# Optimization experiments

Measured on AMD Instinct MI355X. Metric: run time of the kernel, lower is better.

Reference implementation:

```python
import jax, jax.numpy as jnp
import numpy as np

B = 16384        # batch size
D = 128          # embedding dim == ln_bot[-1]
N_EMB = 26       # number of sparse tables
VOCAB = 50000    # rows per table
LN_BOT = [13, 512, 256, 128]
LN_TOP = [479, 1024, 1024, 512, 1]
# triangular indices matching: li=[i for i in range(ni) for j in range(i)] (offset=0, no self-interaction)
LI, LJ = np.tril_indices(N_EMB + 1, -1)


def _init_linear(key, n_in, n_out):
    kw, kb = jax.random.split(key)
    lim = 1.0 / np.sqrt(n_in)
    W = jax.random.uniform(kw, (n_in, n_out), minval=-lim, maxval=lim, dtype=jnp.float32)
    b = jax.random.uniform(kb, (n_out,), minval=-lim, maxval=lim, dtype=jnp.float32)
    return W, b


def setup_inputs() -> dict:
    key = jax.random.key(0)
    ks = jax.random.split(key, 3 + len(LN_BOT) - 1 + len(LN_TOP) - 1)
    inp = {
        "dense_x": jax.random.normal(ks[0], (B, LN_BOT[0]), dtype=jnp.float32),
        "indices": jax.random.randint(ks[1], (N_EMB, B), 0, VOCAB),
        "emb_tables": jax.random.normal(ks[2], (N_EMB, VOCAB, D), dtype=jnp.float32) * 0.01,
    }
    k = 3
    for i in range(len(LN_BOT) - 1):
        W, b = _init_linear(ks[k], LN_BOT[i], LN_BOT[i + 1]); k += 1
        inp[f"bot_W{i}"], inp[f"bot_b{i}"] = W, b
    for i in range(len(LN_TOP) - 1):
        W, b = _init_linear(ks[k], LN_TOP[i], LN_TOP[i + 1]); k += 1
        inp[f"top_W{i}"], inp[f"top_b{i}"] = W, b
    return inp


def reference(dense_x, indices, emb_tables,
              bot_W0, bot_b0, bot_W1, bot_b1, bot_W2, bot_b2,
              top_W0, top_b0, top_W1, top_b1, top_W2, top_b2, top_W3, top_b3):
    # bottom MLP (sigmoid_bot=-1 -> all ReLU)
    x = dense_x
    for W, b in ((bot_W0, bot_b0), (bot_W1, bot_b1), (bot_W2, bot_b2)):
        x = jax.nn.relu(x @ W + b)                      # [B, 128]

    # embedding lookups (bag size 1 per table)
    emb = jax.vmap(lambda t, i: t[i])(emb_tables, indices)   # [26, B, D]
    emb = jnp.transpose(emb, (1, 0, 2))                      # [B, 26, D]

    # dot interaction
    T = jnp.concatenate([x[:, None, :], emb], axis=1)        # [B, 27, D]
    Z = jnp.einsum('bid,bjd->bij', T, T)                     # [B, 27, 27]
    Zflat = Z[:, LI, LJ]                                     # [B, 351]
    R = jnp.concatenate([x, Zflat], axis=1)                  # [B, 479]

    # top MLP (sigmoid on last layer, sigmoid_top=3)
    h = R
    for W, b in ((top_W0, top_b0), (top_W1, top_b1), (top_W2, top_b2)):
        h = jax.nn.relu(h @ W + b)
    p = jax.nn.sigmoid(h @ top_W3 + top_b3)                  # [B, 1]
    return jnp.clip(p, 0.0, 1.0)                             # loss_threshold = 0.0
```

## Files before the change

### kernel.cpp

```cpp
#include <hip/hip_runtime.h>

typedef __attribute__((ext_vector_type(8))) short short8;
typedef __attribute__((ext_vector_type(4))) float f32x4;
typedef __attribute__((ext_vector_type(16))) float f32x16;

#define B_ROWS 16384

__device__ __forceinline__ float bf2f(ushort u){ return __uint_as_float(((uint)u)<<16); }
__device__ __forceinline__ ushort f2bf(float f){
  uint u = __float_as_uint(f);
  u = u + 0x7FFFu + ((u>>16)&1u);
  return (ushort)(u>>16);
}
__device__ __forceinline__ void gload_lds16(const void* g, void* l){
  __builtin_amdgcn_global_load_lds((const __attribute__((address_space(1))) unsigned*)g,
                                   (__attribute__((address_space(3))) unsigned*)l, 16, 0, 0);
}

struct TArgs { const float* in; ushort* out; int K, N, Kp; };
struct TArgs6 { TArgs a[6]; };

__global__ __launch_bounds__(256) void transp_tiled(TArgs6 args)
{
  TArgs t = args.a[blockIdx.z];
  if (t.K == 0){
    if (blockIdx.x==0 && blockIdx.y==0)
      for (int i = threadIdx.x; i < t.N; i += 256) t.out[i] = f2bf(t.in[i]);
    return;
  }
  int k0 = blockIdx.x*32, n0 = blockIdx.y*32;
  if (k0 >= t.Kp || n0 >= t.N) return;
  __shared__ float tile[32][33];
  const int c = threadIdx.x & 31, r8 = threadIdx.x >> 5;
  #pragma unroll
  for (int p=0;p<4;p++){
    int k = k0 + r8 + p*8;
    tile[r8+p*8][c] = (k < t.K) ? t.in[(size_t)k*t.N + n0 + c] : 0.f;
  }
  __syncthreads();
  #pragma unroll
  for (int p=0;p<4;p++){
    int n = n0 + r8 + p*8;
    t.out[(size_t)n*t.Kp + k0 + c] = f2bf(tile[c][r8+p*8]);
  }
}

__global__ __launch_bounds__(256) void bot0(const float* __restrict__ x, const float* __restrict__ W,
                                            const float* __restrict__ bias, ushort* __restrict__ out)
{
  int i = blockIdx.x*256 + threadIdx.x;
  int b = i>>9, n = i&511;
  const float* xr = x + (size_t)b*13;
  float s = bias[n];
  #pragma unroll
  for (int k=0;k<13;k++) s += xr[k]*W[k*512+n];
  out[i] = f2bf(fmaxf(s,0.f));
}

template<int TM, bool RELU>
__global__ __launch_bounds__(256) void gemm_bt(const ushort* __restrict__ A,
    const ushort* __restrict__ Bt, const float* __restrict__ bias,
    ushort* __restrict__ C, int M, int N, int K, int ldc)
{
  constexpr int BM = TM*32;
  __shared__ __align__(16) ushort lA[2][BM*64];
  __shared__ __align__(16) ushort lB[2][128*64];
  const int tid = threadIdx.x;
  const int wave = tid>>6, lane = tid&63;
  const int bm = blockIdx.x*BM, bn = blockIdx.y*128;
  const int wrr = (wave>>1)*(BM/2), wcc = (wave&1)*64;
  const int lr = lane&15, lg = lane>>4;
  const int nt = K>>6;
  const int obA = wave*(TM*1024) + lane*16;
  const int obB = wave*4096 + lane*16;

  f32x4 acc[TM][4];
  #pragma unroll
  for (int m=0;m<TM;m++)
    #pragma unroll
    for (int n=0;n<4;n++)
      #pragma unroll
      for (int j=0;j<4;j++) acc[m][n][j] = 0.f;

  auto stage = [&](int buf, int kt){
    #pragma unroll
    for (int c=0;c<TM;c++){
      int o = obA + c*1024;
      int row = o>>7, colb = o&127;
      gload_lds16((const char*)A  + (((size_t)(bm+row)*K + (kt<<6))<<1) + colb, (char*)lA[buf] + o);
    }
    #pragma unroll
    for (int c=0;c<4;c++){
      int o = obB + c*1024;
      int row = o>>7, colb = o&127;
      gload_lds16((const char*)Bt + (((size_t)(bn+row)*K + (kt<<6))<<1) + colb, (char*)lB[buf] + o);
    }
  };

  stage(0, 0);
  int cur = 0;
  for (int t=0; t<nt; ++t){
    int nx = (t+1 < nt) ? t+1 : 0;
    stage(cur^1, nx);
    if constexpr (TM==4) asm volatile("s_waitcnt vmcnt(8)" ::: "memory");
    else                 asm volatile("s_waitcnt vmcnt(6)" ::: "memory");
    __builtin_amdgcn_s_barrier();
    asm volatile("" ::: "memory");
    #pragma unroll
    for (int kk=0;kk<64;kk+=32){
      short8 af[TM], bfr[4];
      const int lk = kk + lg*8;
      #pragma unroll
      for (int m=0;m<TM;m++) af[m]  = *(const short8*)&lA[cur][(wrr+m*16+lr)*64 + lk];
      #pragma unroll
      for (int n=0;n<4;n++) bfr[n] = *(const short8*)&lB[cur][(wcc+n*16+lr)*64 + lk];
      #pragma unroll
      for (int m=0;m<TM;m++)
        #pragma unroll
        for (int n=0;n<4;n++)
          acc[m][n] = __builtin_amdgcn_mfma_f32_16x16x32_bf16(af[m], bfr[n], acc[m][n], 0,0,0);
    }
    asm volatile("" ::: "memory");
    __builtin_amdgcn_s_barrier();
    cur ^= 1;
  }

  #pragma unroll
  for (int n=0;n<4;n++){
    int col = bn + wcc + n*16 + lr;
    float bv = bias[col];
    #pragma unroll
    for (int m=0;m<TM;m++){
      #pragma unroll
      for (int j=0;j<4;j++){
        int row = bm + wrr + m*16 + lg*4 + j;
        float v = acc[m][n][j] + bv;
        if (RELU) v = fmaxf(v,0.f);
        C[(size_t)row*ldc + col] = f2bf(v);
      }
    }
  }
}

template<int BN>
__global__ __launch_bounds__(512, 2) void gemm256(const ushort* __restrict__ A,
    const ushort* __restrict__ Bt, const float* __restrict__ bias,
    ushort* __restrict__ C, int K, int ldc)
{
  constexpr int  NF = BN/128;
  constexpr int  LB = BN/128;
  constexpr uint BR = (uint)BN*32u;
  constexpr uint BUFSZ = 16384u + 2u*BR;
  __shared__ __align__(16) ushort lds[2*BUFSZ];

  const int tid = threadIdx.x;
  const int wave = tid>>6, lane = tid&63;
  const uint wm = (uint)(wave>>2), wn = (uint)(wave&3);
  const uint lc = (uint)(lane&31), hi = (uint)(lane>>5);
  const int bm = blockIdx.x*256, bn = blockIdx.y*BN;
  const int nt = K>>6, niter = nt>>1;

  f32x16 acc[4][NF];
  #pragma unroll
  for (int m=0;m<4;m++)
    #pragma unroll
    for (int n=0;n<NF;n++)
      #pragma unroll
      for (int j=0;j<16;j++) acc[m][n][j] = 0.f;

  short8 bfr[2][NF];

#define STAGE(MAT, KH, TILE, SBUF) do{                                          \
    int kt_ = (TILE);                                                           \
    int ktc_ = (kt_ < nt) ? kt_ : 0;       \
    const ushort* gb_ = (MAT) ? Bt : A;                                         \
    const uint ro_ = (MAT) ? (uint)bn : (uint)bm;                               \
    const uint rb_ = (uint)(SBUF)*BUFSZ + ((MAT) ? (16384u + (uint)(KH)*BR)     \
                                                 : ((uint)(KH)*8192u));         \
    const int nl_ = (MAT) ? LB : 2;                                             \
    _Pragma("unroll")                                                           \
    for (int j_=0; j_<nl_; ++j_){                                               \
      uint lin_ = (uint)tid*16u + (uint)j_*8192u;                               \
      uint src_ = lin_ ^ (((lin_>>7)&3u)<<4);                                   \
      uint row_ = src_>>6, colb_ = src_&63u;                                    \
      const char* g_ = (const char*)gb_ +                                       \
        (((size_t)(ro_+row_)*(size_t)K + (size_t)ktc_*64 + (KH)*32)<<1) + colb_;\
      gload_lds16(g_, (char*)lds + (size_t)rb_*2 + lin_);                       \
    }                                                                           \
  }while(0)

#define PHASE(CBUF, KKH, MH, BLOAD, SMAT, SKH, STILE, SBUF, CKPT) do{           \
    const uint ab_ = (uint)(CBUF)*BUFSZ + (uint)(KKH)*8192u;                    \
    short8 af_[2][2];                                                           \
    _Pragma("unroll")                                                           \
    for (int mfl_=0; mfl_<2; ++mfl_){                                           \
      uint r_ = wm*128u + ((uint)(MH)*2u+(uint)mfl_)*32u + lc;                  \
      _Pragma("unroll")                                                         \
      for (int k2_=0; k2_<2; ++k2_){                                            \
        uint l_ = r_*64u + hi*16u + (uint)k2_*32u;                              \
        af_[mfl_][k2_] = *(const short8*)((const char*)lds + (size_t)ab_*2      \
                                   + (l_ ^ (((l_>>7)&3u)<<4)));                 \
      }                                                                         \
    }                                                                           \
    if (BLOAD){                                                                 \
      const uint bb_ = (uint)(CBUF)*BUFSZ + 16384u + (uint)(KKH)*BR;            \
      _Pragma("unroll")                                                         \
      for (int nf_=0; nf_<NF; ++nf_){                                           \
        uint r_ = wn*(uint)(BN/4) + (uint)nf_*32u + lc;                         \
        _Pragma("unroll")                                                       \
        for (int k2_=0; k2_<2; ++k2_){                                          \
          uint l_ = r_*64u + hi*16u + (uint)k2_*32u;                            \
          bfr[k2_][nf_] = *(const short8*)((const char*)lds + (size_t)bb_*2     \
                                     + (l_ ^ (((l_>>7)&3u)<<4)));               \
        }                                                                       \
      }                                                                         \
    }                                                                           \
    STAGE(SMAT, SKH, STILE, SBUF);                                              \
    asm volatile("" ::: "memory");                                              \
    __builtin_amdgcn_s_barrier();                                               \
    asm volatile("" ::: "memory");                                              \
    __builtin_amdgcn_s_setprio(1);                                              \
    _Pragma("unroll")                                                           \
    for (int mfl_=0; mfl_<2; ++mfl_)                                            \
      _Pragma("unroll")                                                         \
      for (int nf_=0; nf_<NF; ++nf_)                                            \
        _Pragma("unroll")                                                       \
        for (int k2_=0; k2_<2; ++k2_)                                           \
          acc[(MH)*2+mfl_][nf_] = __builtin_amdgcn_mfma_f32_32x32x16_bf16(      \
              af_[mfl_][k2_], bfr[k2_][nf_], acc[(MH)*2+mfl_][nf_], 0,0,0);     \
    __builtin_amdgcn_s_setprio(0);                                              \
    if (CKPT){                                                                  \
      if constexpr (LB==2) asm volatile("s_waitcnt vmcnt(4)" ::: "memory");     \
      else                 asm volatile("s_waitcnt vmcnt(3)" ::: "memory");     \
    }                                                                           \
    asm volatile("" ::: "memory");                                              \
    __builtin_amdgcn_s_barrier();                                               \
  }while(0)

  STAGE(0,0,0,0); STAGE(1,0,0,0); STAGE(0,1,0,0); STAGE(1,1,0,0);
  STAGE(0,0,1,1); STAGE(1,0,1,1);
  if constexpr (LB==2) asm volatile("s_waitcnt vmcnt(4)" ::: "memory");
  else                 asm volatile("s_waitcnt vmcnt(3)" ::: "memory");
  asm volatile("" ::: "memory");
  __builtin_amdgcn_s_barrier();

  for (int i=0; i<niter; ++i){
    const int O  = 2*i+1;
    const int E2 = 2*i+2;
    const int O2 = 2*i+3;
    PHASE(0,0,0,true , 0,1,O ,1, false);
    PHASE(0,0,1,false, 1,1,O ,1, true );
    PHASE(0,1,0,true , 0,0,E2,0, false);
    PHASE(0,1,1,false, 1,0,E2,0, true );
    PHASE(1,0,0,true , 0,1,E2,0, false);
    PHASE(1,0,1,false, 1,1,E2,0, true );
    PHASE(1,1,0,true , 0,0,O2,1, false);
    PHASE(1,1,1,false, 1,0,O2,1, true );
  }
#undef PHASE
#undef STAGE

  #pragma unroll
  for (int nf=0; nf<NF; ++nf){
    int col = bn + (int)wn*(BN/4) + nf*32 + (int)lc;
    float bv = bias[col];
    #pragma unroll
    for (int mf=0; mf<4; ++mf){
      #pragma unroll
      for (int reg=0; reg<16; ++reg){
        int row = bm + (int)wm*128 + mf*32 + (reg&3) + 8*(reg>>2) + 4*(int)hi;
        float v = acc[mf][nf][reg] + bv;
        C[(size_t)row*ldc + col] = f2bf(fmaxf(v, 0.f));
      }
    }
  }
}

__global__ __launch_bounds__(256) void interact(const int* __restrict__ idx,
    const float* __restrict__ emb, ushort* __restrict__ R)
{
  __shared__ __align__(16) ushort Tl[4][32][136];
  const int w = threadIdx.x>>6, l = threadIdx.x&63;
  const int b = blockIdx.x*4 + w;
  ushort* Rrow = R + (size_t)b*512;

  uint xv = ((const uint*)Rrow)[l];
  *(uint*)&Tl[w][0][2*l] = xv;

  int myidx = (l<26) ? idx[(size_t)l*B_ROWS + b] : 0;
  const int half = l>>5, lc = l&31;
  #pragma unroll
  for (int i=0;i<13;i++){
    const int row = 2*i + 1 + half;
    int e = __shfl(myidx, row - 1);
    const float4* rp = (const float4*)(emb + ((size_t)(row-1)*50000 + (size_t)e)*128);
    float4 v = rp[lc];
    uint2 pk;
    pk.x = (uint)f2bf(v.x) | ((uint)f2bf(v.y)<<16);
    pk.y = (uint)f2bf(v.z) | ((uint)f2bf(v.w)<<16);
    *(uint2*)&Tl[w][row][4*lc] = pk;
  }
  __syncthreads();

  f32x16 acc;
  #pragma unroll
  for (int i=0;i<16;i++) acc[i] = 0.f;
  #pragma unroll
  for (int kk=0;kk<8;kk++){
    short8 fa = *(const short8*)((const char*)&Tl[w][0][0] + (size_t)(l&31)*272 + kk*32 + (l>>5)*16);
    acc = __builtin_amdgcn_mfma_f32_32x32x16_bf16(fa, fa, acc, 0,0,0);
  }

  const int c = l&31;
  #pragma unroll
  for (int j=0;j<16;j++){
    int r = (j&3) + 8*(j>>2) + 4*(l>>5);
    if (c < r && r <= 26) Rrow[128 + r*(r-1)/2 + c] = f2bf(acc[j]);
  }
  if (l < 33) Rrow[479 + l] = 0;
}

__global__ __launch_bounds__(256) void finlayer(const ushort* __restrict__ h3,
    const ushort* __restrict__ wt, const float* __restrict__ b3, float* __restrict__ out)
{
  int w = threadIdx.x>>6, l = threadIdx.x&63;
  int b = blockIdx.x*4 + w;
  short8 hv = *(const short8*)(h3 + (size_t)b*512 + l*8);
  short8 wv = *(const short8*)(wt + l*8);
  float s = 0.f;
  #pragma unroll
  for (int j=0;j<8;j++) s += bf2f((ushort)hv[j])*bf2f((ushort)wv[j]);
  #pragma unroll
  for (int off=32; off>0; off>>=1) s += __shfl_xor(s, off);
  if (l==0){
    float h = s + b3[0];
    float p = 1.f/(1.f + expf(-h));
    out[b] = fminf(fmaxf(p, 0.f), 1.f);
  }
}

extern "C" void kernel_launch(void* const* d_in, const int* in_sizes, int n_in,
                              void* d_out, int out_size, void* d_ws, size_t ws_size,
                              hipStream_t stream)
{
  const float* dense_x = (const float*)d_in[0];
  const int*   indices = (const int*)d_in[1];
  const float* emb     = (const float*)d_in[2];
  const float* bW0 = (const float*)d_in[3];  const float* bb0 = (const float*)d_in[4];
  const float* bW1 = (const float*)d_in[5];  const float* bb1 = (const float*)d_in[6];
  const float* bW2 = (const float*)d_in[7];  const float* bb2 = (const float*)d_in[8];
  const float* tW0 = (const float*)d_in[9];  const float* tb0 = (const float*)d_in[10];
  const float* tW1 = (const float*)d_in[11]; const float* tb1 = (const float*)d_in[12];
  const float* tW2 = (const float*)d_in[13]; const float* tb2 = (const float*)d_in[14];
  const float* tW3 = (const float*)d_in[15]; const float* tb3 = (const float*)d_in[16];
  float* out = (float*)d_out;
  const int Bn = B_ROWS;

  char* ws = (char*)d_ws;
  size_t o = 0;
  auto alloc = [&](size_t bytes)->char*{ char* r = ws + o; o += (bytes + 255) & ~(size_t)255; return r; };
  ushort* wtB1 = (ushort*)alloc(256*512*2);
  ushort* wtB2 = (ushort*)alloc(128*256*2);
  ushort* wtT0 = (ushort*)alloc(1024*512*2);
  ushort* wtT1 = (ushort*)alloc((size_t)1024*1024*2);
  ushort* wtT2 = (ushort*)alloc(512*1024*2);
  ushort* wtT3 = (ushort*)alloc(512*2);
  ushort* P    = (ushort*)alloc((size_t)Bn*512*2);
  ushort* act1 = (ushort*)alloc((size_t)Bn*256*2);
  ushort* h1   = (ushort*)alloc((size_t)Bn*1024*2);
  ushort* h2   = (ushort*)alloc((size_t)Bn*1024*2);
  (void)ws_size; (void)in_sizes; (void)n_in; (void)out_size;

  TArgs6 ta;
  ta.a[0] = { bW1, wtB1, 512 , 256 , 512  };
  ta.a[1] = { bW2, wtB2, 256 , 128 , 256  };
  ta.a[2] = { tW0, wtT0, 479 , 1024, 512  };
  ta.a[3] = { tW1, wtT1, 1024, 1024, 1024 };
  ta.a[4] = { tW2, wtT2, 1024, 512 , 1024 };
  ta.a[5] = { tW3, wtT3, 0   , 512 , 0    };
  transp_tiled<<<dim3(32,32,6),256,0,stream>>>(ta);

  bot0<<<Bn*512/256,256,0,stream>>>(dense_x, bW0, bb0, P);
  gemm_bt<4,true><<<dim3(128,2),256,0,stream>>>(P,    wtB1, bb1, act1, Bn,256,512, 256);
  gemm_bt<2,true><<<dim3(256,1),256,0,stream>>>(act1, wtB2, bb2, P,    Bn,128,256, 512);

  interact<<<Bn/4,256,0,stream>>>(indices, emb, P);

  gemm256<256><<<dim3(64,4),512,0,stream>>>(P,  wtT0, tb0, h1, 512 , 1024);
  gemm256<256><<<dim3(64,4),512,0,stream>>>(h1, wtT1, tb1, h2, 1024, 1024);
  gemm256<128><<<dim3(64,4),512,0,stream>>>(h2, wtT2, tb2, P,  1024, 512);
  finlayer<<<Bn/4,256,0,stream>>>(P, wtT3, tb3, out);
}
```

Baseline: 197.0 us.

## Fuse final dot layer into last GEMM epilogue and merge prep kernels

Merges the weight-transpose kernel and the first bottom-MLP layer into one prep kernel that also zeroes a partial-sum buffer. The last top-MLP GEMM now applies bias and ReLU, multiplies by the final-layer weight, reduces across lanes and atomically adds into per-row partials. A small sigmoid kernel then finishes the output. This avoids writing and re-reading the 16384x512 activation and saves launches, at the cost of float atomics (order-dependent sums) and a shuffle reduction in the epilogue.

After: 197.2 us. No clear change (+0.1%).

```diff
diff --git a/kernel.cpp b/kernel.cpp
--- a/kernel.cpp
+++ b/kernel.cpp
@@ -18,43 +18,53 @@
 }
 
 struct TArgs { const float* in; ushort* out; int K, N, Kp; };
-struct TArgs6 { TArgs a[6]; };
-
-__global__ __launch_bounds__(256) void transp_tiled(TArgs6 args)
-{
-  TArgs t = args.a[blockIdx.z];
-  if (t.K == 0){
-    if (blockIdx.x==0 && blockIdx.y==0)
-      for (int i = threadIdx.x; i < t.N; i += 256) t.out[i] = f2bf(t.in[i]);
+struct PrepArgs {
+  const float* x; const float* W0; const float* b0; ushort* act0;
+  TArgs t[5];
+  float* partial;
+};
+
+__global__ __launch_bounds__(256) void prep(PrepArgs a)
+{
+  const int idx = blockIdx.x;
+  const int tid = threadIdx.x;
+  __shared__ float tile[32][33];
+
+  if (idx < 32768){
+    int i = idx*256 + tid;
+    int b = i>>9, n = i&511;
+    const float* xr = a.x + (size_t)b*13;
+    float s = a.b0[n];
+    #pragma unroll
+    for (int k=0;k<13;k++) s += xr[k]*a.W0[k*512+n];
+    a.act0[i] = f2bf(fmaxf(s,0.f));
     return;
   }
-  int k0 = blockIdx.x*32, n0 = blockIdx.y*32;
-  if (k0 >= t.Kp || n0 >= t.N) return;
-  __shared__ float tile[32][33];
-  const int c = threadIdx.x & 31, r8 = threadIdx.x >> 5;
+  if (idx >= 34976){
+    a.partial[(idx-34976)*256 + tid] = 0.f;
+    return;
+  }
+  int t = idx - 32768, s;
+  int kx, ny;
+  if (t < 128)            { s=0; kx=t%16; ny=t/16; }
+  else if ((t-=128) < 32) { s=1; kx=t%8 ; ny=t/8 ; }
+  else if ((t-=32) < 512) { s=2; kx=t%16; ny=t/16; }
+  else if ((t-=512)<1024) { s=3; kx=t%32; ny=t/32; }
+  else                    { s=4; kx=(t-1024)%32; ny=(t-1024)/32; }
+  TArgs ta = a.t[s];
+  int k0 = kx*32, n0 = ny*32;
+  const int c = tid & 31, r8 = tid >> 5;
   #pragma unroll
   for (int p=0;p<4;p++){
     int k = k0 + r8 + p*8;
-    tile[r8+p*8][c] = (k < t.K) ? t.in[(size_t)k*t.N + n0 + c] : 0.f;
+    tile[r8+p*8][c] = (k < ta.K) ? ta.in[(size_t)k*ta.N + n0 + c] : 0.f;
   }
   __syncthreads();
   #pragma unroll
   for (int p=0;p<4;p++){
     int n = n0 + r8 + p*8;
-    t.out[(size_t)n*t.Kp + k0 + c] = f2bf(tile[c][r8+p*8]);
-  }
-}
-
-__global__ __launch_bounds__(256) void bot0(const float* __restrict__ x, const float* __restrict__ W,
-                                            const float* __restrict__ bias, ushort* __restrict__ out)
-{
-  int i = blockIdx.x*256 + threadIdx.x;
-  int b = i>>9, n = i&511;
-  const float* xr = x + (size_t)b*13;
-  float s = bias[n];
-  #pragma unroll
-  for (int k=0;k<13;k++) s += xr[k]*W[k*512+n];
-  out[i] = f2bf(fmaxf(s,0.f));
+    ta.out[(size_t)n*ta.Kp + k0 + c] = f2bf(tile[c][r8+p*8]);
+  }
 }
 
 template<int TM, bool RELU>
@@ -142,10 +152,11 @@
   }
 }
 
-template<int BN>
+template<int BN, bool FUSE>
 __global__ __launch_bounds__(512, 2) void gemm256(const ushort* __restrict__ A,
     const ushort* __restrict__ Bt, const float* __restrict__ bias,
-    ushort* __restrict__ C, int K, int ldc)
+    ushort* __restrict__ C, int K, int ldc,
+    const float* __restrict__ w3, float* __restrict__ partial)
 {
   constexpr int  NF = BN/128;
   constexpr int  LB = BN/128;
@@ -260,17 +271,36 @@
 #undef PHASE
 #undef STAGE
 
-  #pragma unroll
-  for (int nf=0; nf<NF; ++nf){
-    int col = bn + (int)wn*(BN/4) + nf*32 + (int)lc;
+  if constexpr (FUSE){
+    int col = bn + (int)wn*(BN/4) + (int)lc;
     float bv = bias[col];
+    float wv = w3[col];
     #pragma unroll
     for (int mf=0; mf<4; ++mf){
       #pragma unroll
       for (int reg=0; reg<16; ++reg){
-        int row = bm + (int)wm*128 + mf*32 + (reg&3) + 8*(reg>>2) + 4*(int)hi;
-        float v = acc[mf][nf][reg] + bv;
-        C[(size_t)row*ldc + col] = f2bf(fmaxf(v, 0.f));
+        float v = fmaxf(acc[mf][0][reg] + bv, 0.f) * wv;
+        #pragma unroll
+        for (int off=1; off<32; off<<=1) v += __shfl_xor(v, off);
+        if (lc == 0){
+          int row = bm + (int)wm*128 + mf*32 + (reg&3) + 8*(reg>>2) + 4*(int)hi;
+          atomicAdd(&partial[row], v);
+        }
+      }
+    }
+  } else {
+    #pragma unroll
+    for (int nf=0; nf<NF; ++nf){
+      int col = bn + (int)wn*(BN/4) + nf*32 + (int)lc;
+      float bv = bias[col];
+      #pragma unroll
+      for (int mf=0; mf<4; ++mf){
+        #pragma unroll
+        for (int reg=0; reg<16; ++reg){
+          int row = bm + (int)wm*128 + mf*32 + (reg&3) + 8*(reg>>2) + 4*(int)hi;
+          float v = acc[mf][nf][reg] + bv;
+          C[(size_t)row*ldc + col] = f2bf(fmaxf(v, 0.f));
+        }
       }
     }
   }
@@ -320,23 +350,13 @@
   if (l < 33) Rrow[479 + l] = 0;
 }
 
-__global__ __launch_bounds__(256) void finlayer(const ushort* __restrict__ h3,
-    const ushort* __restrict__ wt, const float* __restrict__ b3, float* __restrict__ out)
-{
-  int w = threadIdx.x>>6, l = threadIdx.x&63;
-  int b = blockIdx.x*4 + w;
-  short8 hv = *(const short8*)(h3 + (size_t)b*512 + l*8);
-  short8 wv = *(const short8*)(wt + l*8);
-  float s = 0.f;
-  #pragma unroll
-  for (int j=0;j<8;j++) s += bf2f((ushort)hv[j])*bf2f((ushort)wv[j]);
-  #pragma unroll
-  for (int off=32; off>0; off>>=1) s += __shfl_xor(s, off);
-  if (l==0){
-    float h = s + b3[0];
-    float p = 1.f/(1.f + expf(-h));
-    out[b] = fminf(fmaxf(p, 0.f), 1.f);
-  }
+__global__ __launch_bounds__(256) void sigm(const float* __restrict__ partial,
+    const float* __restrict__ b3, float* __restrict__ out)
+{
+  int i = blockIdx.x*256 + threadIdx.x;
+  float h = partial[i] + b3[0];
+  float p = 1.f/(1.f + expf(-h));
+  out[i] = fminf(fmaxf(p, 0.f), 1.f);
 }
 
 extern "C" void kernel_launch(void* const* d_in, const int* in_sizes, int n_in,
@@ -364,30 +384,30 @@
   ushort* wtT0 = (ushort*)alloc(1024*512*2);
   ushort* wtT1 = (ushort*)alloc((size_t)1024*1024*2);
   ushort* wtT2 = (ushort*)alloc(512*1024*2);
-  ushort* wtT3 = (ushort*)alloc(512*2);
+  float*  partial = (float*)alloc(B_ROWS*4);
   ushort* P    = (ushort*)alloc((size_t)Bn*512*2);
   ushort* act1 = (ushort*)alloc((size_t)Bn*256*2);
   ushort* h1   = (ushort*)alloc((size_t)Bn*1024*2);
   ushort* h2   = (ushort*)alloc((size_t)Bn*1024*2);
   (void)ws_size; (void)in_sizes; (void)n_in; (void)out_size;
 
-  TArgs6 ta;
-  ta.a[0] = { bW1, wtB1, 512 , 256 , 512  };
-  ta.a[1] = { bW2, wtB2, 256 , 128 , 256  };
-  ta.a[2] = { tW0, wtT0, 479 , 1024, 512  };
-  ta.a[3] = { tW1, wtT1, 1024, 1024, 1024 };
-  ta.a[4] = { tW2, wtT2, 1024, 512 , 1024 };
-  ta.a[5] = { tW3, wtT3, 0   , 512 , 0    };
-  transp_tiled<<<dim3(32,32,6),256,0,stream>>>(ta);
-
-  bot0<<<Bn*512/256,256,0,stream>>>(dense_x, bW0, bb0, P);
+  PrepArgs pa;
+  pa.x = dense_x; pa.W0 = bW0; pa.b0 = bb0; pa.act0 = P;
+  pa.t[0] = { bW1, wtB1, 512 , 256 , 512  };
+  pa.t[1] = { bW2, wtB2, 256 , 128 , 256  };
+  pa.t[2] = { tW0, wtT0, 479 , 1024, 512  };
+  pa.t[3] = { tW1, wtT1, 1024, 1024, 1024 };
+  pa.t[4] = { tW2, wtT2, 1024, 512 , 1024 };
+  pa.partial = partial;
+  prep<<<35040,256,0,stream>>>(pa);
+
   gemm_bt<4,true><<<dim3(128,2),256,0,stream>>>(P,    wtB1, bb1, act1, Bn,256,512, 256);
   gemm_bt<2,true><<<dim3(256,1),256,0,stream>>>(act1, wtB2, bb2, P,    Bn,128,256, 512);
 
   interact<<<Bn/4,256,0,stream>>>(indices, emb, P);
 
-  gemm256<256><<<dim3(64,4),512,0,stream>>>(P,  wtT0, tb0, h1, 512 , 1024);
-  gemm256<256><<<dim3(64,4),512,0,stream>>>(h1, wtT1, tb1, h2, 1024, 1024);
-  gemm256<128><<<dim3(64,4),512,0,stream>>>(h2, wtT2, tb2, P,  1024, 512);
-  finlayer<<<Bn/4,256,0,stream>>>(P, wtT3, tb3, out);
-}
+  gemm256<256,false><<<dim3(64,4),512,0,stream>>>(P,  wtT0, tb0, h1, 512 , 1024, nullptr, nullptr);
+  gemm256<256,false><<<dim3(64,4),512,0,stream>>>(h1, wtT1, tb1, h2, 1024, 1024, nullptr, nullptr);
+  gemm256<128,true ><<<dim3(64,4),512,0,stream>>>(h2, wtT2, tb2, nullptr, 1024, 0, tW3, partial);
+  sigm<<<Bn/256,256,0,stream>>>(partial, tb3, out);
+}
```
